# Performance work log

Hardware: AMD Instinct MI355X
Metric: run time of the kernel (lower is better)

## Reference

```python
import jax, jax.numpy as jnp
import numpy as np
import math


def ste_round(x):
    # round with straight-through gradient (identity in bwd)
    return x + jax.lax.stop_gradient(jnp.round(x) - x)


def ste_floor(x):
    return x + jax.lax.stop_gradient(jnp.floor(x) - x)


def _conv(x, w, b):
    # 5x5 stride-2 conv, padding=2 (kernel_size//2), NCHW/OIHW
    y = jax.lax.conv_general_dilated(
        x, w, window_strides=(2, 2), padding=[(2, 2), (2, 2)],
        dimension_numbers=('NCHW', 'OIHW', 'NCHW'))
    return y + b[None, :, None, None]


def _split_conv(x, w, b_int, mul, split=4):
    # 4 redundant sub-convolutions with floor-STE quantized integer weights/biases
    wq = ste_round(w)  # wSTE: round-to-int with STE
    out = 0.0
    for i in range(split):
        out = out + _conv(x, ste_floor((wq + i) / split), ste_floor((b_int + i) / split))
    return out * mul[None, :, None, None]


def _forward(x, w0, b0, w1, b1, w2, b2, w3, b3, mul0, mul1, mul2, mul3,
             relu0, relu1, relu2, md0, md1, md2, md3, ga_left):
    Bits = 8; clp_k = 8; in_scale = 8; scl_k = 3
    relus = [relu0, relu1, relu2]
    clp = [round((2 ** Bits - 1) / r * 2 ** (16 + clp_k)) for r in relus]
    scl = [math.floor((r + 2 ** (scl_k - 1)) / 2 ** scl_k) for r in relus]

    # quantize input to uint8 range
    x = jnp.clip(ste_round(x * 2 ** in_scale), 0, 255)

    # ---- layer 0 ----
    x = _split_conv(x, w0, ste_round(b0 * 2 ** in_scale), mul0)
    x = ste_floor((x + 2.0 ** (md0 - 1 + in_scale - clp_k)) / 2.0 ** (md0 + in_scale - clp_k))
    x = jnp.clip(x, 0, clp[0])
    x = ste_floor((ste_round(x * scl[0]) + 2.0 ** (15 + clp_k - scl_k)) / 2.0 ** (16 + clp_k - scl_k))

    # ---- layers 1, 2 ----
    for w_, b_, mul_, md_, idx in ((w1, b1, mul1, md1, 1), (w2, b2, mul2, md2, 2)):
        x = _split_conv(x, w_, ste_round(b_), mul_)
        x = ste_floor((x + 2.0 ** (md_ - 1 - clp_k)) / 2.0 ** (md_ - clp_k))
        x = jnp.clip(x, 0, clp[idx])
        x = ste_floor((ste_round(x * scl[idx]) + 2.0 ** (15 + clp_k - scl_k)) / 2.0 ** (16 + clp_k - scl_k))

    # ---- layer 3 (latent) ----
    x = _split_conv(x, w3, ste_round(b3), mul3)
    x = ste_floor((x + 2.0 ** (md3 - 1 - ga_left)) / 2.0 ** (md3 - ga_left))
    return x


def setup_inputs():
    key = jax.random.key(0)
    ks = jax.random.split(key, 16)
    N, M = 192, 320
    d = {}
    d['x'] = jax.random.uniform(ks[0], (4, 3, 512, 512), dtype=jnp.float32)
    # float weights whose round() gives small ints (integerized LIC weights)
    d['w0'] = jax.random.normal(ks[1], (N, 3, 5, 5), dtype=jnp.float32) * 3.0
    d['b0'] = jax.random.normal(ks[2], (N,), dtype=jnp.float32)
    d['w1'] = jax.random.normal(ks[3], (N, N, 5, 5), dtype=jnp.float32) * 3.0
    d['b1'] = jax.random.normal(ks[4], (N,), dtype=jnp.float32) * 16.0
    d['w2'] = jax.random.normal(ks[5], (N, N, 5, 5), dtype=jnp.float32) * 3.0
    d['b2'] = jax.random.normal(ks[6], (N,), dtype=jnp.float32) * 16.0
    d['w3'] = jax.random.normal(ks[7], (M, N, 5, 5), dtype=jnp.float32) * 3.0
    d['b3'] = jax.random.normal(ks[8], (M,), dtype=jnp.float32) * 16.0
    # per-channel integer-valued fixed-point multipliers
    d['mul0'] = jax.random.randint(ks[9], (N,), 1, 64).astype(jnp.float32)
    d['mul1'] = jax.random.randint(ks[10], (N,), 1, 64).astype(jnp.float32)
    d['mul2'] = jax.random.randint(ks[11], (N,), 1, 64).astype(jnp.float32)
    d['mul3'] = jax.random.randint(ks[12], (M,), 1, 64).astype(jnp.float32)
    d['relu0'] = 65536; d['relu1'] = 65536; d['relu2'] = 65536
    d['md0'] = 7; d['md1'] = 15; d['md2'] = 15; d['md3'] = 10
    d['ga_left'] = 4
    return d


def reference(x, w0, b0, w1, b1, w2, b2, w3, b3, mul0, mul1, mul2, mul3,
              relu0, relu1, relu2, md0, md1, md2, md3, ga_left):
    return _forward(x, w0, b0, w1, b1, w2, b2, w3, b3, mul0, mul1, mul2, mul3,
                    relu0, relu1, relu2, md0, md1, md2, md3, ga_left)
```

## Files before the change

### kernel.cpp

```cpp
#include <hip/hip_runtime.h>
#include <hip/hip_bf16.h>

typedef int i32x4 __attribute__((ext_vector_type(4)));
typedef unsigned int u32;
typedef unsigned long long u64;
typedef long long ll;

__device__ __forceinline__ void load_lds16(const void* g, void* l) {
  __builtin_amdgcn_global_load_lds(
      (const __attribute__((address_space(1))) u32*)g,
      (__attribute__((address_space(3))) u32*)l, 16, 0, 0);
}

__global__ __launch_bounds__(256) void prep_all(
    const float* __restrict__ w0, const float* __restrict__ w1,
    const float* __restrict__ w2, const float* __restrict__ w3,
    signed char* __restrict__ w0q, signed char* __restrict__ w1p,
    signed char* __restrict__ w2p, signed char* __restrict__ w3p,
    signed char* __restrict__ zbuf,
    int* __restrict__ totw0, int* __restrict__ totw1,
    int* __restrict__ totw2, int* __restrict__ totw3)
{
  __shared__ signed char ldsw[8 * 4800];
  const int blk = blockIdx.x;
  const int tid = threadIdx.x;

  if (blk < 88) {
    const float* wsrc; signed char* wdst; int* tot; int MF, sub;
    if (blk < 24)      { wsrc = w1; wdst = w1p; tot = totw1; MF = 12; sub = blk; }
    else if (blk < 48) { wsrc = w2; wdst = w2p; tot = totw2; MF = 12; sub = blk - 24; }
    else               { wsrc = w3; wdst = w3p; tot = totw3; MF = 20; sub = blk - 48; }
    const int mf = sub >> 1, half = sub & 1, colbase = half * 8;
    const int ocb = mf * 16 + colbase;
    for (int o = 0; o < 8; o++) {
      const float* src = wsrc + (size_t)(ocb + o) * 4800;
      int s = 0;
      for (int j = tid; j < 4800; j += 256) {
        int v = (int)rintf(src[j]);
        ldsw[o * 4800 + j] = (signed char)v;
        s += v;
      }
      atomicAdd(&tot[ocb + o], s);
    }
    __syncthreads();
    for (int u = tid; u < 9600; u += 256) {
      int eu = u & 3, colL = (u >> 2) & 7, q = (u >> 5) & 3, t = u >> 7;
      int tap = t / 3, ch = t - 3 * tap;
      int ci0 = ch * 64 + q * 16 + eu * 4;
      const signed char* sp = ldsw + colL * 4800 + tap;
      u32 wv = 0;
      #pragma unroll
      for (int bb = 0; bb < 4; bb++)
        wv |= ((u32)(unsigned char)sp[(ci0 + bb) * 25]) << (8 * bb);
      *(u32*)(wdst + ((size_t)t * MF + mf) * 1024 +
              (q * 16 + colbase + colL) * 16 + eu * 4) = wv;
    }
  } else {
    if (tid < 128) ((u64*)zbuf)[tid] = 0x8080808080808080ULL;
    for (int i = tid; i < 24576; i += 256) {
      int e = i & 15, colA = (i >> 4) & 15, q = (i >> 8) & 3, t = i >> 10;
      int mf = t % 12, ch = t / 12;
      signed char v = 0;
      if (e < 15 && (ch == 0 || q == 0)) {
        int ky = (ch == 0) ? q : 4;
        int ci = e / 5, kx = e - ci * 5;
        v = (signed char)(int)rintf(
            w0[((mf * 16 + colA) * 3 + ci) * 25 + ky * 5 + kx]);
      }
      w0q[i] = v;
    }
    for (int oc = tid; oc < 192; oc += 256) {
      const float* p = w0 + (size_t)oc * 75;
      int s = 0;
      #pragma unroll 5
      for (int j = 0; j < 75; j++) s += (int)rintf(p[j]);
      totw0[oc] = s;
    }
  }
}

__global__ __launch_bounds__(192, 3) void conv0F(
    const float* __restrict__ x, const signed char* __restrict__ wq,
    const float* __restrict__ bias, const float* __restrict__ mulv,
    const int* __restrict__ totw,
    const int* __restrict__ reluP, const int* __restrict__ mdP,
    unsigned char* __restrict__ outA)
{
  __shared__ signed char ilds[3][5][132];

  const int tid = threadIdx.x;
  const int lane = tid & 63;
  const int col = lane & 15;
  const int quad = lane >> 4;
  const int w = tid >> 6;
  const int blk = blockIdx.x;
  const int oxblk = blk & 3;
  const int oy = (blk >> 2) & 255;
  const int b = blk >> 10;
  const int oxbase = oxblk * 64;

  i32x4 afr[2][4];
  #pragma unroll
  for (int ch = 0; ch < 2; ch++)
    #pragma unroll
    for (int i = 0; i < 4; i++)
      afr[ch][i] = *(const i32x4*)(wq + ch * 12288 + (w * 4 + i) * 1024 + lane * 16);

  const float* xb = x + (size_t)b * 3 * 512 * 512;
  for (int i = tid; i < 990; i += 192) {
    int j = i % 66; int t = i / 66; int r = t % 5; int ci = t / 5;
    int iy = 2 * oy - 2 + r;
    int ix = 2 * oxbase - 2 + 2 * j;
    int v0 = -128, v1 = -128;
    if ((unsigned)iy < 512u) {
      const float* row = xb + ((size_t)ci * 512 + iy) * 512;
      if ((unsigned)ix < 512u) {
        float xv = rintf(row[ix] * 256.0f);
        v0 = (int)fminf(fmaxf(xv, 0.0f), 255.0f) - 128;
      }
      if ((unsigned)(ix + 1) < 512u) {
        float xv = rintf(row[ix + 1] * 256.0f);
        v1 = (int)fminf(fmaxf(xv, 0.0f), 255.0f) - 128;
      }
    }
    *(unsigned short*)&ilds[ci][r][2 * j] =
        (unsigned short)((v0 & 0xFF) | ((v1 & 0xFF) << 8));
  }
  __syncthreads();

  i32x4 acc[4][4];
  #pragma unroll
  for (int fm = 0; fm < 4; fm++)
    #pragma unroll
    for (int fn = 0; fn < 4; fn++) acc[fm][fn] = (i32x4){0, 0, 0, 0};

  #pragma unroll
  for (int ch = 0; ch < 2; ch++) {
    const int row = (ch == 0) ? quad : 4;
    i32x4 bfr[4];
    #pragma unroll
    for (int fn = 0; fn < 4; fn++) {
      const int xb2 = 2 * (fn * 16 + col);
      const int o8 = (xb2 & 3) * 8;
      const int ab = xb2 & ~3;
      u64 w0_, w1_, w2_;
      {
        const u32* p0 = (const u32*)&ilds[0][row][ab];
        const u32* p1 = (const u32*)&ilds[1][row][ab];
        const u32* p2 = (const u32*)&ilds[2][row][ab];
        w0_ = (u64)p0[0] | ((u64)p0[1] << 32);
        w1_ = (u64)p1[0] | ((u64)p1[1] << 32);
        w2_ = (u64)p2[0] | ((u64)p2[1] << 32);
      }
      u32 a0 = (u32)(w0_ >> o8);
      u32 a1 = ((u32)(w0_ >> (o8 + 32)) & 0xFFu) | (((u32)(w1_ >> o8)) << 8);
      u32 a2 = ((u32)(w1_ >> (o8 + 24)) & 0xFFFFu) | (((u32)(w2_ >> o8)) << 16);
      u32 a3 = (u32)(w2_ >> (o8 + 16));
      bfr[fn] = (i32x4){(int)a0, (int)a1, (int)a2, (int)a3};
    }
    #pragma unroll
    for (int fm = 0; fm < 4; fm++)
      #pragma unroll
      for (int fn = 0; fn < 4; fn++)
        acc[fm][fn] = __builtin_amdgcn_mfma_i32_16x16x64_i8(
            afr[ch][fm], bfr[fn], acc[fm][fn], 0, 0, 0);
  }

  const size_t pix0 = ((size_t)(b * 256 + oy)) * 256 + oxbase;
  const int rl = reluP[0];
  const int sh = mdP[0];
  const ll clpv_ll = llrint(255.0 / (double)rl * 16777216.0);
  const int clpv = clpv_ll > 0x7FFFFFFFLL ? 0x7FFFFFFF : (int)clpv_ll;
  const int sclv = (int)((rl + 4) >> 3);
  const int rnd = 1 << (sh - 1);
  #pragma unroll
  for (int fm = 0; fm < 4; fm++) {
    const int oc0 = w * 64 + fm * 16 + quad * 4;
    int bim[4], mu32[4];
    #pragma unroll
    for (int r = 0; r < 4; r++) {
      int bi = (int)llrintf(bias[oc0 + r] * 256.0f) + 128 * totw[oc0 + r];
      mu32[r] = (int)llrintf(mulv[oc0 + r]);
      bim[r] = bi * mu32[r];
    }
    #pragma unroll
    for (int fn = 0; fn < 4; fn++) {
      const size_t pix = pix0 + fn * 16 + col;
      u32 wd = 0;
      #pragma unroll
      for (int r = 0; r < 4; r++) {
        int vi = acc[fm][fn][r] * mu32[r] + bim[r];
        int y = (vi + rnd) >> sh;
        y = y < 0 ? 0 : (y > clpv ? clpv : y);
        y = (y * sclv + (1 << 20)) >> 21;
        wd |= (((u32)y ^ 0x80u) & 0xFFu) << (8 * r);
      }
      *(u32*)(outA + pix * 192 + oc0) = wd;
    }
  }
}

template <int COUT, int HIN, int WIN, int HOUT, int WOUT, int MW,
          int KSPLIT, bool DIRECT, int NH>
__global__ __launch_bounds__((MW + 1) * 64, 2) void convS(
    const signed char* __restrict__ act, const signed char* __restrict__ wp,
    const float* __restrict__ bias, const float* __restrict__ mulv,
    const int* __restrict__ totw,
    const int* __restrict__ reluP, const int* __restrict__ mdP,
    const signed char* __restrict__ zbuf,
    unsigned char* __restrict__ outA, int* __restrict__ outP)
{
  constexpr int CIN = 192;
  constexpr int PASSES = 4;
  constexpr int SAe = MW * 4096;
  constexpr int TX = WOUT / (16 * NH);
  constexpr int TYB = HOUT / 4;
  constexpr int TPP = 25 / KSPLIT;
  constexpr int NSTEP = TPP * 3;
  constexpr int NB = 4 * NH;
  constexpr int BUFB = NB * 1024;
  constexpr int PSZ = 4 * HOUT * WOUT * COUT;
  static_assert(MW * 64 == COUT, "M covers COUT");
  static_assert(NSTEP >= 4, "pipeline depth");

  __shared__ __align__(16) char smem[4 * BUFB];

  const int tid = threadIdx.x;
  const int lane = tid & 63;
  const int col = lane & 15;
  const int quad = lane >> 4;
  const int w = tid >> 6;
  const int part = blockIdx.y;

  int bx = blockIdx.x;
  const int tx = bx % TX; bx /= TX;
  const int ty = bx % TYB;
  const int b = bx / TYB;
  const int ox0 = tx * 16 * NH;
  const int oy0 = ty * 4;
  const int tap0 = part * TPP;

  if (w == MW) {
    const signed char* bptr[PASSES * NH];
    int bmxh[NH], bmy[PASSES];
    #pragma unroll
    for (int h = 0; h < NH; h++) {
      const int oxv = ox0 + h * 16 + col;
      int mx = 0;
      #pragma unroll
      for (int kk = 0; kk < 5; kk++)
        if ((unsigned)(2 * oxv + kk - 2) < (unsigned)WIN) mx |= 1 << kk;
      bmxh[h] = mx;
    }
    #pragma unroll
    for (int p = 0; p < PASSES; p++) {
      const int oyv = oy0 + p;
      int my = 0;
      #pragma unroll
      for (int kk = 0; kk < 5; kk++)
        if ((unsigned)(2 * oyv + kk - 2) < (unsigned)HIN) my |= 1 << kk;
      bmy[p] = my;
      #pragma unroll
      for (int h = 0; h < NH; h++) {
        const int oxv = ox0 + h * 16 + col;
        bptr[p * NH + h] =
            act + ((size_t)b * HIN * WIN + (size_t)(2 * oyv) * WIN + 2 * oxv) * CIN
            + quad * 16;
      }
    }
    int kyS = tap0 / 5, kxS = tap0 - 5 * kyS, chS = 0;
    auto stage = [&](int sel) {
      const int offB = ((kyS - 2) * WIN + (kxS - 2)) * CIN + chS * 64;
      #pragma unroll
      for (int p = 0; p < PASSES; p++)
        #pragma unroll
        for (int h = 0; h < NH; h++) {
          bool v = ((bmxh[h] >> kxS) & 1) && ((bmy[p] >> kyS) & 1);
          const signed char* g = v ? (bptr[p * NH + h] + offB) : (zbuf + quad * 16);
          load_lds16(g, smem + sel * BUFB + (p * NH + h) * 1024);
        }
      chS++;
      if (chS == 3) { chS = 0; kxS++; if (kxS == 5) { kxS = 0; kyS++; } }
    };
    stage(0); stage(1); stage(2);
    if constexpr (NH == 2) asm volatile("s_waitcnt vmcnt(16)" ::: "memory");
    else                   asm volatile("s_waitcnt vmcnt(8)" ::: "memory");
    asm volatile("s_barrier" ::: "memory");
    #pragma unroll 1
    for (int sl = 0; sl + 1 < NSTEP; ++sl) {
      if (sl + 3 < NSTEP) stage((sl + 3) & 3);
      const int rem = NSTEP - 2 - sl;
      if constexpr (NH == 2) {
        if (rem >= 2)      asm volatile("s_waitcnt vmcnt(16)" ::: "memory");
        else if (rem == 1) asm volatile("s_waitcnt vmcnt(8)" ::: "memory");
        else               asm volatile("s_waitcnt vmcnt(0)" ::: "memory");
      } else {
        if (rem >= 2)      asm volatile("s_waitcnt vmcnt(8)" ::: "memory");
        else if (rem == 1) asm volatile("s_waitcnt vmcnt(4)" ::: "memory");
        else               asm volatile("s_waitcnt vmcnt(0)" ::: "memory");
      }
      asm volatile("s_barrier" ::: "memory");
    }
    return;
  }

  i32x4 acc[4][NB];
  #pragma unroll
  for (int fm = 0; fm < 4; fm++)
    #pragma unroll
    for (int j = 0; j < NB; j++) acc[fm][j] = (i32x4){0, 0, 0, 0};

  const signed char* aptr = wp + (size_t)(tap0 * 3) * SAe + w * 4096 + lane * 16;
  i32x4 aA[4], aB[4];
  #pragma unroll
  for (int i = 0; i < 4; i++) aA[i] = *(const i32x4*)(aptr + i * 1024);

  auto comp = [&](int base, i32x4 (&a)[4]) {
    const char* pB = smem + base + lane * 16;
    i32x4 bfr[NB];
    #pragma unroll
    for (int i = 0; i < NB; i++)
      bfr[i] = *(const i32x4*)(pB + i * 1024);
    #pragma unroll
    for (int fm = 0; fm < 4; fm++)
      #pragma unroll
      for (int j = 0; j < NB; j++)
        acc[fm][j] = __builtin_amdgcn_mfma_i32_16x16x64_i8(
            a[fm], bfr[j], acc[fm][j], 0, 0, 0);
  };

  asm volatile("s_barrier" ::: "memory");
  int sl = 0;
  #pragma unroll 1
  for (; sl + 1 < NSTEP; sl += 2) {
    aptr += SAe;
    #pragma unroll
    for (int i = 0; i < 4; i++) aB[i] = *(const i32x4*)(aptr + i * 1024);
    comp((sl & 3) * BUFB, aA);
    asm volatile("s_barrier" ::: "memory");
    if (sl + 2 < NSTEP) {
      aptr += SAe;
      #pragma unroll
      for (int i = 0; i < 4; i++) aA[i] = *(const i32x4*)(aptr + i * 1024);
    }
    comp(((sl + 1) & 3) * BUFB, aB);
    if (sl + 2 < NSTEP) asm volatile("s_barrier" ::: "memory");
  }
  if (sl < NSTEP) {
    comp((sl & 3) * BUFB, aA);
  }

  if constexpr (DIRECT) {
    const int rl = reluP[0];
    const int sh = mdP[0] - 8;
    const ll clpv = llrint(255.0 / (double)rl * 16777216.0);
    const ll sclv = (ll)((rl + 4) >> 3);
    #pragma unroll
    for (int fm = 0; fm < 4; fm++) {
      const int oc0 = w * 64 + fm * 16 + quad * 4;
      ll bi[4], mu[4];
      #pragma unroll
      for (int r = 0; r < 4; r++) {
        bi[r] = llrintf(bias[oc0 + r]) + 128LL * totw[oc0 + r];
        mu[r] = llrintf(mulv[oc0 + r]);
      }
      #pragma unroll
      for (int j = 0; j < NB; j++) {
        const int p = j / NH, h = j % NH;
        const int oyv = oy0 + p;
        const int oxv = ox0 + h * 16 + col;
        u32 wd = 0;
        #pragma unroll
        for (int r = 0; r < 4; r++) {
          ll vi = ((ll)acc[fm][j][r] + bi[r]) * mu[r];
          ll y = (vi + (1LL << (sh - 1))) >> sh;
          y = y < 0 ? 0LL : (y > clpv ? clpv : y);
          y = (y * sclv + (1LL << 20)) >> 21;
          wd |= (((u32)y ^ 0x80u) & 0xFFu) << (8 * r);
        }
        *(u32*)(outA + ((size_t)((b * HOUT + oyv) * WOUT + oxv)) * COUT + oc0) = wd;
      }
    }
  } else {
    int* pout = outP + (size_t)part * PSZ;
    #pragma unroll
    for (int fm = 0; fm < 4; fm++) {
      const int oc0 = w * 64 + fm * 16 + quad * 4;
      #pragma unroll
      for (int j = 0; j < NB; j++) {
        const int p = j / NH, h = j % NH;
        const int oyv = oy0 + p;
        const int oxv = ox0 + h * 16 + col;
        *(i32x4*)(pout + ((size_t)((b * HOUT + oyv) * WOUT + oxv)) * COUT + oc0) =
            acc[fm][j];
      }
    }
  }
}

__global__ __launch_bounds__(256) void reduce2(
    const int* __restrict__ partP, const float* __restrict__ bias,
    const float* __restrict__ mulv, const int* __restrict__ totw,
    const int* __restrict__ reluP, const int* __restrict__ mdP,
    unsigned char* __restrict__ outA)
{
  const int gid = blockIdx.x * 256 + threadIdx.x;
  const int PSZ4 = 4 * 64 * 64 * 192 / 4;
  const int4* pp = (const int4*)partP;
  int4 sv = pp[gid];
  #pragma unroll
  for (int p = 1; p < 5; p++) {
    int4 v = pp[(size_t)p * PSZ4 + gid];
    sv.x += v.x; sv.y += v.y; sv.z += v.z; sv.w += v.w;
  }
  int sa[4] = {sv.x, sv.y, sv.z, sv.w};
  const int oc0 = (gid * 4) % 192;
  const int rl = reluP[0];
  const int sh = mdP[0] - 8;
  const ll clpv = llrint(255.0 / (double)rl * 16777216.0);
  const ll sclv = (ll)((rl + 4) >> 3);
  u32 wd = 0;
  #pragma unroll
  for (int r = 0; r < 4; r++) {
    ll bi = llrintf(bias[oc0 + r]) + 128LL * totw[oc0 + r];
    ll mu = llrintf(mulv[oc0 + r]);
    ll vi = ((ll)sa[r] + bi) * mu;
    ll y = (vi + (1LL << (sh - 1))) >> sh;
    y = y < 0 ? 0LL : (y > clpv ? clpv : y);
    y = (y * sclv + (1LL << 20)) >> 21;
    wd |= (((u32)y ^ 0x80u) & 0xFFu) << (8 * r);
  }
  ((u32*)outA)[gid] = wd;
}

__global__ __launch_bounds__(256) void reduce3(
    const int* __restrict__ partP, const float* __restrict__ b3,
    const float* __restrict__ mul3, const int* __restrict__ totw3,
    const int* __restrict__ mdP, const int* __restrict__ gaP,
    float* __restrict__ outF)
{
  const int gid = blockIdx.x * 256 + threadIdx.x;
  int t = gid;
  const int ox = t & 31; t >>= 5;
  const int oy = t & 31; t >>= 5;
  const int oc = t % 320;
  const int b  = t / 320;
  const int PSZ = 4 * 32 * 32 * 320;
  const size_t src = ((size_t)((b * 32 + oy) * 32 + ox)) * 320 + oc;
  ll s = 0;
  #pragma unroll
  for (int p = 0; p < 5; p++) s += partP[(size_t)p * PSZ + src];
  const int sh = mdP[0] - gaP[0];
  const ll bi = llrintf(b3[oc]) + 128LL * totw3[oc];
  const ll mu = llrintf(mul3[oc]);
  const ll y = ((s + bi) * mu + (1LL << (sh - 1))) >> sh;
  outF[gid] = (float)y;
}

extern "C" void kernel_launch(void* const* d_in, const int* in_sizes, int n_in,
                              void* d_out, int out_size, void* d_ws, size_t ws_size,
                              hipStream_t stream)
{
  const float* x    = (const float*)d_in[0];
  const float* w0   = (const float*)d_in[1];
  const float* b0   = (const float*)d_in[2];
  const float* w1   = (const float*)d_in[3];
  const float* b1   = (const float*)d_in[4];
  const float* w2   = (const float*)d_in[5];
  const float* b2   = (const float*)d_in[6];
  const float* w3   = (const float*)d_in[7];
  const float* b3   = (const float*)d_in[8];
  const float* mul0 = (const float*)d_in[9];
  const float* mul1 = (const float*)d_in[10];
  const float* mul2 = (const float*)d_in[11];
  const float* mul3 = (const float*)d_in[12];
  const int* relu0  = (const int*)d_in[13];
  const int* relu1  = (const int*)d_in[14];
  const int* relu2  = (const int*)d_in[15];
  const int* md0    = (const int*)d_in[16];
  const int* md1    = (const int*)d_in[17];
  const int* md2    = (const int*)d_in[18];
  const int* md3    = (const int*)d_in[19];
  const int* ga     = (const int*)d_in[20];

  char* ws = (char*)d_ws;
  size_t off = 0;
  signed char* zbuf = (signed char*)(ws + off); off += 1024;
  signed char* w0q  = (signed char*)(ws + off); off += 24576;
  signed char* w1p  = (signed char*)(ws + off); off += 921600;
  signed char* w2p  = (signed char*)(ws + off); off += 921600;
  signed char* w3p  = (signed char*)(ws + off); off += 1536000;
  int*         totw1= (int*)        (ws + off); off += 192 * 4;
  int*         totw2= (int*)        (ws + off); off += 192 * 4;
  int*         totw3= (int*)        (ws + off); off += 320 * 4;
  int*         totw0= (int*)        (ws + off); off += 192 * 4;
  unsigned char* act1 = (unsigned char*)(ws + off); off += (size_t)4 * 256 * 256 * 192;
  unsigned char* act2 = (unsigned char*)(ws + off); off += (size_t)4 * 128 * 128 * 192;
  unsigned char* act3 = (unsigned char*)(ws + off); off += (size_t)4 * 64 * 64 * 192;
  int*         partl  = (int*)(ws + off); off += (size_t)5 * 4 * 64 * 64 * 192 * 4;
  (void)ws_size; (void)in_sizes; (void)n_in; (void)out_size;

  hipMemsetAsync(totw1, 0, (192 + 192 + 320 + 192) * 4, stream);
  prep_all<<<89, 256, 0, stream>>>(w0, w1, w2, w3, w0q, w1p, w2p, w3p,
                                   zbuf, totw0, totw1, totw2, totw3);
  conv0F<<<4096, 192, 0, stream>>>(x, w0q, b0, mul0, totw0, relu0, md0, act1);
  convS<192, 256, 256, 128, 128, 3, 1, true, 2><<<dim3(512, 1), 256, 0, stream>>>(
      (const signed char*)act1, w1p, b1, mul1, totw1, relu1, md1, zbuf, act2, nullptr);
  convS<192, 128, 128, 64, 64, 3, 5, false, 2><<<dim3(128, 5), 256, 0, stream>>>(
      (const signed char*)act2, w2p, b2, mul2, totw2, relu2, md2, zbuf, nullptr, partl);
  reduce2<<<3072, 256, 0, stream>>>(partl, b2, mul2, totw2, relu2, md2, act3);
  convS<320, 64, 64, 32, 32, 5, 5, false, 1><<<dim3(64, 5), 384, 0, stream>>>(
      (const signed char*)act3, w3p, b3, mul3, totw3, nullptr, md3, zbuf, nullptr, partl);
  reduce3<<<5120, 256, 0, stream>>>(partl, b3, mul3, totw3, md3, ga, (float*)d_out);
}
```

Before: 324.1 us.

## Replace dedicated loader wave with cooperative loading across all compute waves

Drops the producer/consumer split in the strided conv kernel. Before, one wave issued global-to-LDS activation loads while the others ran MFMAs. Now every wave issues a share of the activation tile loads, interleaved with its own weight loads and MFMA steps, and the output channels are split across more waves (4 for the 192-channel layers, 5 for the latent layer). The aim is to put more waves on matrix work for the same block size and spread the memory issue cost. In exchange, each wave carries extra load-issue work and more complex vmcnt and barrier reasoning inside the compute loop.

```diff
diff --git a/kernel.cpp b/kernel.cpp
--- a/kernel.cpp
+++ b/kernel.cpp
@@ -200,9 +200,9 @@
   }
 }
 
-template <int COUT, int HIN, int WIN, int HOUT, int WOUT, int MW,
+template <int COUT, int HIN, int WIN, int HOUT, int WOUT, int WV,
           int KSPLIT, bool DIRECT, int NH>
-__global__ __launch_bounds__((MW + 1) * 64, 2) void convS(
+__global__ __launch_bounds__(WV * 64, 2) void convS(
     const signed char* __restrict__ act, const signed char* __restrict__ wp,
     const float* __restrict__ bias, const float* __restrict__ mulv,
     const int* __restrict__ totw,
@@ -212,15 +212,19 @@
 {
   constexpr int CIN = 192;
   constexpr int PASSES = 4;
-  constexpr int SAe = MW * 4096;
+  constexpr int MF = COUT / 16;
+  constexpr int OCW = COUT / WV;
+  constexpr int FM = OCW / 16;
+  constexpr int SAe = MF * 1024;
   constexpr int TX = WOUT / (16 * NH);
   constexpr int TYB = HOUT / 4;
   constexpr int TPP = 25 / KSPLIT;
   constexpr int NSTEP = TPP * 3;
-  constexpr int NB = 4 * NH;
+  constexpr int NB = PASSES * NH;
   constexpr int BUFB = NB * 1024;
+  constexpr int SMAX = (NB + WV - 1) / WV;
   constexpr int PSZ = 4 * HOUT * WOUT * COUT;
-  static_assert(MW * 64 == COUT, "M covers COUT");
+  static_assert(WV * OCW == COUT, "M covers COUT");
   static_assert(NSTEP >= 4, "pipeline depth");
 
   __shared__ __align__(16) char smem[4 * BUFB];
@@ -240,109 +244,87 @@
   const int oy0 = ty * 4;
   const int tap0 = part * TPP;
 
-  if (w == MW) {
-    const signed char* bptr[PASSES * NH];
-    int bmxh[NH], bmy[PASSES];
-    #pragma unroll
-    for (int h = 0; h < NH; h++) {
+  const signed char* bp[SMAX];
+  int mjx[SMAX], mjy[SMAX];
+  #pragma unroll
+  for (int k = 0; k < SMAX; k++) {
+    const int j = w + k * WV;
+    if (j < NB) {
+      const int p = j / NH, h = j % NH;
       const int oxv = ox0 + h * 16 + col;
-      int mx = 0;
-      #pragma unroll
-      for (int kk = 0; kk < 5; kk++)
+      const int oyv = oy0 + p;
+      bp[k] = act + ((size_t)b * HIN * WIN + (size_t)(2 * oyv) * WIN + 2 * oxv) * CIN
+              + quad * 16;
+      int mx = 0, my = 0;
+      #pragma unroll
+      for (int kk = 0; kk < 5; kk++) {
         if ((unsigned)(2 * oxv + kk - 2) < (unsigned)WIN) mx |= 1 << kk;
-      bmxh[h] = mx;
-    }
-    #pragma unroll
-    for (int p = 0; p < PASSES; p++) {
-      const int oyv = oy0 + p;
-      int my = 0;
-      #pragma unroll
-      for (int kk = 0; kk < 5; kk++)
         if ((unsigned)(2 * oyv + kk - 2) < (unsigned)HIN) my |= 1 << kk;
-      bmy[p] = my;
-      #pragma unroll
-      for (int h = 0; h < NH; h++) {
-        const int oxv = ox0 + h * 16 + col;
-        bptr[p * NH + h] =
-            act + ((size_t)b * HIN * WIN + (size_t)(2 * oyv) * WIN + 2 * oxv) * CIN
-            + quad * 16;
-      }
-    }
-    int kyS = tap0 / 5, kxS = tap0 - 5 * kyS, chS = 0;
-    auto stage = [&](int sel) {
-      const int offB = ((kyS - 2) * WIN + (kxS - 2)) * CIN + chS * 64;
-      #pragma unroll
-      for (int p = 0; p < PASSES; p++)
-        #pragma unroll
-        for (int h = 0; h < NH; h++) {
-          bool v = ((bmxh[h] >> kxS) & 1) && ((bmy[p] >> kyS) & 1);
-          const signed char* g = v ? (bptr[p * NH + h] + offB) : (zbuf + quad * 16);
-          load_lds16(g, smem + sel * BUFB + (p * NH + h) * 1024);
-        }
-      chS++;
-      if (chS == 3) { chS = 0; kxS++; if (kxS == 5) { kxS = 0; kyS++; } }
-    };
-    stage(0); stage(1); stage(2);
-    if constexpr (NH == 2) asm volatile("s_waitcnt vmcnt(16)" ::: "memory");
-    else                   asm volatile("s_waitcnt vmcnt(8)" ::: "memory");
-    asm volatile("s_barrier" ::: "memory");
-    #pragma unroll 1
-    for (int sl = 0; sl + 1 < NSTEP; ++sl) {
-      if (sl + 3 < NSTEP) stage((sl + 3) & 3);
-      const int rem = NSTEP - 2 - sl;
-      if constexpr (NH == 2) {
-        if (rem >= 2)      asm volatile("s_waitcnt vmcnt(16)" ::: "memory");
-        else if (rem == 1) asm volatile("s_waitcnt vmcnt(8)" ::: "memory");
-        else               asm volatile("s_waitcnt vmcnt(0)" ::: "memory");
-      } else {
-        if (rem >= 2)      asm volatile("s_waitcnt vmcnt(8)" ::: "memory");
-        else if (rem == 1) asm volatile("s_waitcnt vmcnt(4)" ::: "memory");
-        else               asm volatile("s_waitcnt vmcnt(0)" ::: "memory");
-      }
-      asm volatile("s_barrier" ::: "memory");
-    }
-    return;
-  }
-
-  i32x4 acc[4][NB];
-  #pragma unroll
-  for (int fm = 0; fm < 4; fm++)
+      }
+      mjx[k] = mx; mjy[k] = my;
+    }
+  }
+  int kyS = tap0 / 5, kxS = tap0 - 5 * kyS, chS = 0;
+  auto stage = [&](int sel) {
+    const int offB = ((kyS - 2) * WIN + (kxS - 2)) * CIN + chS * 64;
+    #pragma unroll
+    for (int k = 0; k < SMAX; k++) {
+      const int j = w + k * WV;
+      if (j < NB) {
+        bool v = ((mjx[k] >> kxS) & 1) && ((mjy[k] >> kyS) & 1);
+        const signed char* g = v ? (bp[k] + offB) : (zbuf + quad * 16);
+        load_lds16(g, smem + sel * BUFB + j * 1024);
+      }
+    }
+    chS++;
+    if (chS == 3) { chS = 0; kxS++; if (kxS == 5) { kxS = 0; kyS++; } }
+  };
+
+  i32x4 acc[FM][NB];
+  #pragma unroll
+  for (int fm = 0; fm < FM; fm++)
     #pragma unroll
     for (int j = 0; j < NB; j++) acc[fm][j] = (i32x4){0, 0, 0, 0};
 
-  const signed char* aptr = wp + (size_t)(tap0 * 3) * SAe + w * 4096 + lane * 16;
-  i32x4 aA[4], aB[4];
-  #pragma unroll
-  for (int i = 0; i < 4; i++) aA[i] = *(const i32x4*)(aptr + i * 1024);
-
-  auto comp = [&](int base, i32x4 (&a)[4]) {
+  const signed char* aptr = wp + (size_t)(tap0 * 3) * SAe + w * FM * 1024 + lane * 16;
+  i32x4 aA[FM], aB[FM];
+  #pragma unroll
+  for (int i = 0; i < FM; i++) aA[i] = *(const i32x4*)(aptr + i * 1024);
+
+  auto comp = [&](int base, i32x4 (&a)[FM]) {
     const char* pB = smem + base + lane * 16;
     i32x4 bfr[NB];
     #pragma unroll
     for (int i = 0; i < NB; i++)
       bfr[i] = *(const i32x4*)(pB + i * 1024);
     #pragma unroll
-    for (int fm = 0; fm < 4; fm++)
+    for (int fm = 0; fm < FM; fm++)
       #pragma unroll
       for (int j = 0; j < NB; j++)
         acc[fm][j] = __builtin_amdgcn_mfma_i32_16x16x64_i8(
             a[fm], bfr[j], acc[fm][j], 0, 0, 0);
   };
 
+  stage(0); stage(1); stage(2);
+  if constexpr (SMAX == 2) asm volatile("s_waitcnt vmcnt(4)" ::: "memory");
+  else                     asm volatile("s_waitcnt vmcnt(2)" ::: "memory");
   asm volatile("s_barrier" ::: "memory");
+
   int sl = 0;
   #pragma unroll 1
   for (; sl + 1 < NSTEP; sl += 2) {
     aptr += SAe;
     #pragma unroll
-    for (int i = 0; i < 4; i++) aB[i] = *(const i32x4*)(aptr + i * 1024);
+    for (int i = 0; i < FM; i++) aB[i] = *(const i32x4*)(aptr + i * 1024);
+    if (sl + 3 < NSTEP) stage((sl + 3) & 3);
     comp((sl & 3) * BUFB, aA);
     asm volatile("s_barrier" ::: "memory");
     if (sl + 2 < NSTEP) {
       aptr += SAe;
       #pragma unroll
-      for (int i = 0; i < 4; i++) aA[i] = *(const i32x4*)(aptr + i * 1024);
-    }
+      for (int i = 0; i < FM; i++) aA[i] = *(const i32x4*)(aptr + i * 1024);
+    }
+    if (sl + 4 < NSTEP) stage((sl + 4) & 3);
     comp(((sl + 1) & 3) * BUFB, aB);
     if (sl + 2 < NSTEP) asm volatile("s_barrier" ::: "memory");
   }
@@ -356,8 +338,8 @@
     const ll clpv = llrint(255.0 / (double)rl * 16777216.0);
     const ll sclv = (ll)((rl + 4) >> 3);
     #pragma unroll
-    for (int fm = 0; fm < 4; fm++) {
-      const int oc0 = w * 64 + fm * 16 + quad * 4;
+    for (int fm = 0; fm < FM; fm++) {
+      const int oc0 = w * OCW + fm * 16 + quad * 4;
       ll bi[4], mu[4];
       #pragma unroll
       for (int r = 0; r < 4; r++) {
@@ -384,8 +366,8 @@
   } else {
     int* pout = outP + (size_t)part * PSZ;
     #pragma unroll
-    for (int fm = 0; fm < 4; fm++) {
-      const int oc0 = w * 64 + fm * 16 + quad * 4;
+    for (int fm = 0; fm < FM; fm++) {
+      const int oc0 = w * OCW + fm * 16 + quad * 4;
       #pragma unroll
       for (int j = 0; j < NB; j++) {
         const int p = j / NH, h = j % NH;
@@ -504,12 +486,12 @@
   prep_all<<<89, 256, 0, stream>>>(w0, w1, w2, w3, w0q, w1p, w2p, w3p,
                                    zbuf, totw0, totw1, totw2, totw3);
   conv0F<<<4096, 192, 0, stream>>>(x, w0q, b0, mul0, totw0, relu0, md0, act1);
-  convS<192, 256, 256, 128, 128, 3, 1, true, 2><<<dim3(512, 1), 256, 0, stream>>>(
+  convS<192, 256, 256, 128, 128, 4, 1, true, 2><<<dim3(512, 1), 256, 0, stream>>>(
       (const signed char*)act1, w1p, b1, mul1, totw1, relu1, md1, zbuf, act2, nullptr);
-  convS<192, 128, 128, 64, 64, 3, 5, false, 2><<<dim3(128, 5), 256, 0, stream>>>(
+  convS<192, 128, 128, 64, 64, 4, 5, false, 2><<<dim3(128, 5), 256, 0, stream>>>(
       (const signed char*)act2, w2p, b2, mul2, totw2, relu2, md2, zbuf, nullptr, partl);
   reduce2<<<3072, 256, 0, stream>>>(partl, b2, mul2, totw2, relu2, md2, act3);
-  convS<320, 64, 64, 32, 32, 5, 5, false, 1><<<dim3(64, 5), 384, 0, stream>>>(
+  convS<320, 64, 64, 32, 32, 5, 5, false, 1><<<dim3(64, 5), 320, 0, stream>>>(
       (const signed char*)act3, w3p, b3, mul3, totw3, nullptr, md3, zbuf, nullptr, partl);
   reduce3<<<5120, 256, 0, stream>>>(partl, b3, mul3, totw3, md3, ga, (float*)d_out);
 }
```

New measurement: 332.5 us. +2.6%, slower.
